# Kernel optimization log

Measured on AMD Instinct MI355X. Metric: run time of the kernel, lower is better.

The kernel has to match this reference:

```python
import jax, jax.numpy as jnp
import numpy as np

H, D_HEAD, MEM, K_OUT, J_DIM = 4, 16, 64, 192, 256
LN_EPS = 1e-5

def setup_inputs() -> dict:
    key = jax.random.key(0)
    ks = jax.random.split(key, 12)
    B, T, P = 4, 2048, 16
    inp = {
        "joint_repr": jax.random.normal(ks[0], (B, T, P, J_DIM), jnp.float32),
        "curvature": jax.random.uniform(ks[1], (B,), jnp.float32),
        "entropy": jax.random.uniform(ks[2], (B,), jnp.float32),
        "Wq": 0.02 * jax.random.normal(ks[3], (MEM, J_DIM), jnp.float32),
        "Wk": 0.02 * jax.random.normal(ks[4], (MEM, J_DIM), jnp.float32),
        "Wv": 0.02 * jax.random.normal(ks[5], (MEM, J_DIM), jnp.float32),
        "Wbeta_w": 0.05 * jax.random.normal(ks[6], (H, J_DIM), jnp.float32),
        "Wbeta_b": jnp.full((H,), 0.5, jnp.float32),
        "Walpha_w": 0.05 * jax.random.normal(ks[7], (H, J_DIM), jnp.float32),
        "Walpha_b": jnp.full((H,), -1.0, jnp.float32),
        "curv_w": 0.001 * jax.random.normal(ks[8], (H, 1), jnp.float32),
        "ent_w": 0.001 * jax.random.normal(ks[9], (H, 1), jnp.float32),
        "out_w": 0.01 * jax.random.normal(ks[10], (K_OUT, MEM), jnp.float32),
        "out_b": jnp.zeros((K_OUT,), jnp.float32),
        "ln_q_w": jnp.ones((D_HEAD,), jnp.float32),
        "ln_q_b": jnp.zeros((D_HEAD,), jnp.float32),
        "ln_k_w": jnp.ones((D_HEAD,), jnp.float32),
        "ln_k_b": jnp.zeros((D_HEAD,), jnp.float32),
    }
    return inp

def _ln(y, w, b):
    m = jnp.mean(y, axis=-1, keepdims=True)
    var = jnp.mean((y - m) ** 2, axis=-1, keepdims=True)
    return (y - m) / jnp.sqrt(var + LN_EPS) * w + b

def reference(joint_repr, curvature, entropy, Wq, Wk, Wv, Wbeta_w, Wbeta_b,
              Walpha_w, Walpha_b, curv_w, ent_w, out_w, out_b,
              ln_q_w, ln_q_b, ln_k_w, ln_k_b):
    B, T, P, J = joint_repr.shape
    N = B * P
    x = joint_repr.reshape(N, T, J)  # matches torch reshape(B*P, T, J)
    q = _ln((x @ Wq.T).reshape(N, T, H, D_HEAD), ln_q_w, ln_q_b)
    k = _ln((x @ Wk.T).reshape(N, T, H, D_HEAD), ln_k_w, ln_k_b)
    v = (x @ Wv.T).reshape(N, T, H, D_HEAD)
    k = k / jnp.clip(jnp.linalg.norm(k, axis=-1, keepdims=True), 1e-12)
    beta = jax.nn.sigmoid(x @ Wbeta_w.T + Wbeta_b)    # (N,T,H)
    alpha = jax.nn.sigmoid(x @ Walpha_w.T + Walpha_b)  # (N,T,H)
    # curvature modulation (detached in original)
    Kv = jnp.clip(jnp.abs(jax.lax.stop_gradient(curvature)), None, 10.0)
    Kv = jnp.repeat(Kv, P)  # (N,)
    beta = jax.nn.sigmoid(beta + Kv[:, None, None] * curv_w[:, 0])
    # entropy modulation (detached)
    Sv = jnp.clip(jax.lax.stop_gradient(entropy), 0.0, 5.0)
    Sv = jnp.repeat(Sv, P)
    alpha = jax.nn.sigmoid(alpha + Sv[:, None, None] * ent_w[:, 0])

    def step(M, inps):
        k_t, v_t, q_t, b_t, a_t = inps  # (N,H,d), (N,H)
        Mk = jnp.einsum('nhij,nhj->nhi', M, k_t)
        outer_kk = Mk[..., :, None] * k_t[..., None, :]
        outer_vk = v_t[..., :, None] * k_t[..., None, :]
        M = M - a_t[:, :, None, None] * outer_kk + b_t[:, :, None, None] * outer_vk
        o = jnp.einsum('nhij,nhj->nhi', M, q_t)
        return M, o

    M0 = jnp.zeros((N, H, D_HEAD, D_HEAD), joint_repr.dtype)
    xs = (k.transpose(1, 0, 2, 3), v.transpose(1, 0, 2, 3), q.transpose(1, 0, 2, 3),
          beta.transpose(1, 0, 2), alpha.transpose(1, 0, 2))
    _, outs = jax.lax.scan(step, M0, xs)  # (T,N,H,d)
    out = outs.transpose(1, 0, 2, 3).reshape(N, T, H * D_HEAD)
    fib = out @ out_w.T + out_b  # (N,T,K)
    return fib.reshape(B, P, T, K_OUT).transpose(0, 2, 1, 3)  # (B,T,P,K)
```

## Files before the change

### kernel.cpp

```cpp
#include <hip/hip_runtime.h>

#define TDIM 2048
#define SEG 16
#define SEGLEN 128

typedef __attribute__((ext_vector_type(8))) short short8;
typedef __attribute__((ext_vector_type(4))) short short4v;
typedef __attribute__((ext_vector_type(4))) float float4v;

__device__ __forceinline__ float sigf(float x) { return 1.0f / (1.0f + __expf(-x)); }

__device__ __forceinline__ unsigned short f2bf_rne(float f) {
    unsigned u = __float_as_uint(f);
    unsigned r = (u + 0x7fffu + ((u >> 16) & 1u)) >> 16;
    return (unsigned short)r;
}
__device__ __forceinline__ float bf2f(unsigned short h) {
    return __uint_as_float(((unsigned)h) << 16);
}
struct bfpair { short hi, lo; };
__device__ __forceinline__ bfpair cvt_split(float x) {
    bfpair p;
    unsigned short h = f2bf_rne(x);
    p.hi = (short)h;
    p.lo = (short)f2bf_rne(x - bf2f(h));
    return p;
}

__device__ __forceinline__ void split4_fast(float4 v, short4v& hi, short4v& lo) {
    unsigned h01, h23;
    asm("v_cvt_pk_bf16_f32 %0, %1, %2" : "=v"(h01) : "v"(v.x), "v"(v.y));
    asm("v_cvt_pk_bf16_f32 %0, %1, %2" : "=v"(h23) : "v"(v.z), "v"(v.w));
    float rx = v.x - __uint_as_float(h01 << 16);
    float ry = v.y - __uint_as_float(h01 & 0xffff0000u);
    float rz = v.z - __uint_as_float(h23 << 16);
    float rw = v.w - __uint_as_float(h23 & 0xffff0000u);
    unsigned l01, l23;
    asm("v_cvt_pk_bf16_f32 %0, %1, %2" : "=v"(l01) : "v"(rx), "v"(ry));
    asm("v_cvt_pk_bf16_f32 %0, %1, %2" : "=v"(l23) : "v"(rz), "v"(rw));
    union { unsigned u[2]; short4v s; } uh, ul;
    uh.u[0] = h01; uh.u[1] = h23;
    ul.u[0] = l01; ul.u[1] = l23;
    hi = uh.s; lo = ul.s;
}

template<int CTRL>
__device__ __forceinline__ float dpp_addt(float v) {
    int t = __builtin_amdgcn_update_dpp(0, __float_as_int(v), CTRL, 0xf, 0xf, true);
    return v + __int_as_float(t);
}
__device__ __forceinline__ float red16d(float v) {
    v = dpp_addt<0xB1>(v);
    v = dpp_addt<0x4E>(v);
    v = dpp_addt<0x141>(v);
    v = dpp_addt<0x140>(v);
    return v;
}

__device__ __forceinline__ float dot4f(float4 a, float4 b) {
    return fmaf(a.w, b.w, fmaf(a.z, b.z, fmaf(a.y, b.y, a.x * b.x)));
}
__device__ __forceinline__ float red4g(float v) {
    v += __shfl_xor(v, 16);
    v += __shfl_xor(v, 32);
    return v;
}

__device__ __forceinline__ void gld16(const void* g, void* l) {
    __builtin_amdgcn_global_load_lds(
        (const __attribute__((address_space(1))) unsigned*)g,
        (__attribute__((address_space(3))) unsigned*)l, 16, 0, 0);
}

__global__ __launch_bounds__(256) void prep_w_kernel(
    const float* __restrict__ Wq, const float* __restrict__ Wk, const float* __restrict__ Wv,
    const float* __restrict__ Wbw, const float* __restrict__ Waw,
    short* __restrict__ wimg)
{
    int u = blockIdx.x * 256 + threadIdx.x;
    if (u >= 6656) return;
    int kc = u / 1664, rem = u % 1664;
    int rr = rem >> 3, gg = rem & 7;
    const float* wrow = nullptr;
    if (rr < 64)       wrow = Wq  + (size_t)rr * 256;
    else if (rr < 128) wrow = Wk  + (size_t)(rr - 64) * 256;
    else if (rr < 192) wrow = Wv  + (size_t)(rr - 128) * 256;
    else if (rr < 196) wrow = Wbw + (size_t)(rr - 192) * 256;
    else if (rr < 200) wrow = Waw + (size_t)(rr - 196) * 256;
    int usw = (2 * gg) ^ (rr & 7);
    short* dh = wimg + ((size_t)kc * 3328 + rr * 16 + usw) * 8;
    short* dl = wimg + ((size_t)kc * 3328 + rr * 16 + (usw ^ 1)) * 8;
#pragma unroll
    for (int s = 0; s < 8; ++s) {
        float v = wrow ? wrow[kc * 64 + gg * 8 + s] : 0.0f;
        bfpair p = cvt_split(v);
        dh[s] = p.hi; dl[s] = p.lo;
    }
}

__global__ __launch_bounds__(256) void prep_ow_kernel(
    const float* __restrict__ ow, short* __restrict__ owimg)
{
    int u = blockIdx.x * 256 + threadIdx.x;
    if (u >= 1536) return;
    int rr = u >> 3, gg = u & 7;
    int usw = (2 * gg) ^ (rr & 7);
    short* dh = owimg + ((size_t)rr * 16 + usw) * 8;
    short* dl = owimg + ((size_t)rr * 16 + (usw ^ 1)) * 8;
#pragma unroll
    for (int s = 0; s < 8; ++s) {
        bfpair p = cvt_split(ow[(size_t)rr * 64 + gg * 8 + s]);
        dh[s] = p.hi; dl[s] = p.lo;
    }
}

__global__ __launch_bounds__(256, 2) void proj_kernel(
    const float* __restrict__ x, const float* __restrict__ curv, const float* __restrict__ ent,
    const short* __restrict__ wimg,
    const float* __restrict__ Wbb, const float* __restrict__ Wab,
    const float* __restrict__ cw, const float* __restrict__ ew,
    const float* __restrict__ lnqw, const float* __restrict__ lnqb,
    const float* __restrict__ lnkw, const float* __restrict__ lnkb,
    float* __restrict__ q_ws, float* __restrict__ k_ws, float* __restrict__ v_ws,
    float* __restrict__ beta_ws, float* __restrict__ alpha_ws)
{
    __shared__ __align__(16) short xsh[64 * 128];
    __shared__ __align__(16) short wsh[208 * 128];

    const int tid = threadIdx.x;
    const int lane = tid & 63, wv = tid >> 6;
    const int i16 = lane & 15, gq = lane >> 4, swz = i16 & 7;
    const int row0 = blockIdx.x * 64;
    const int ntbase = (wv == 0) ? 0 : (1 + 3 * wv);
    const int ntcnt  = (wv == 0) ? 4 : 3;

    float4v acc[4][4];
#pragma unroll
    for (int m = 0; m < 4; ++m)
#pragma unroll
        for (int nI = 0; nI < 4; ++nI) acc[m][nI] = (float4v){0.f, 0.f, 0.f, 0.f};

    float4 xr[4];
#pragma unroll
    for (int it = 0; it < 4; ++it) {
        int f = it * 256 + tid, rr = f >> 4, c4 = f & 15;
        xr[it] = *(const float4*)&x[(size_t)(row0 + rr) * 256 + c4 * 4];
    }

#pragma unroll
    for (int kc = 0; kc < 4; ++kc) {
        __builtin_amdgcn_s_barrier();
        const short* wsrc = wimg + (size_t)kc * 26624;
#pragma unroll
        for (int it = 0; it < 13; ++it) {
            int f = it * 256 + tid;
            gld16(wsrc + (size_t)f * 8, &wsh[f * 8]);
        }
        asm volatile("" ::: "memory");
#pragma unroll
        for (int it = 0; it < 4; ++it) {
            int f = it * 256 + tid, rr = f >> 4, c4 = f & 15;
            short4v hi, lo;
            split4_fast(xr[it], hi, lo);
            int usw = (2 * (c4 >> 1)) ^ (rr & 7);
            *(short4v*)&xsh[rr * 128 + usw * 8 + (c4 & 1) * 4] = hi;
            *(short4v*)&xsh[rr * 128 + (usw ^ 1) * 8 + (c4 & 1) * 4] = lo;
        }
        if (kc < 3) {
#pragma unroll
            for (int it = 0; it < 4; ++it) {
                int f = it * 256 + tid, rr = f >> 4, c4 = f & 15;
                xr[it] = *(const float4*)&x[(size_t)(row0 + rr) * 256 + (kc + 1) * 64 + c4 * 4];
            }
            asm volatile("s_waitcnt vmcnt(4) lgkmcnt(0)" ::: "memory");
        } else {
            asm volatile("s_waitcnt vmcnt(0) lgkmcnt(0)" ::: "memory");
        }
        __builtin_amdgcn_s_barrier();
#pragma unroll
        for (int ks = 0; ks < 2; ++ks) {
            const int g4 = ks * 4 + gq;
            const int uA = ((2 * g4) ^ swz) * 8;
            short8 ah[4], al[4];
#pragma unroll
            for (int m = 0; m < 4; ++m) {
                const int rb = (m * 16 + i16) * 128;
                ah[m] = *(const short8*)&xsh[rb + uA];
                al[m] = *(const short8*)&xsh[rb + (uA ^ 8)];
            }
#pragma unroll
            for (int nI = 0; nI < 4; ++nI) if (nI < ntcnt) {
                const int rowB = ((ntbase + nI) * 16 + i16) * 128;
                short8 bh = *(const short8*)&wsh[rowB + uA];
                short8 bl = *(const short8*)&wsh[rowB + (uA ^ 8)];
#pragma unroll
                for (int m = 0; m < 4; ++m) {
                    acc[m][nI] = __builtin_amdgcn_mfma_f32_16x16x32_bf16(ah[m], bh, acc[m][nI], 0, 0, 0);
                    acc[m][nI] = __builtin_amdgcn_mfma_f32_16x16x32_bf16(ah[m], bl, acc[m][nI], 0, 0, 0);
                    acc[m][nI] = __builtin_amdgcn_mfma_f32_16x16x32_bf16(al[m], bh, acc[m][nI], 0, 0, 0);
                }
            }
        }
    }

    const int c = i16;
    const float lnqw_c = lnqw[c], lnqb_c = lnqb[c];
    const float lnkw_c = lnkw[c], lnkb_c = lnkb[c];
    const int nblk = row0 >> 11;
    const float Kv = fminf(fabsf(curv[nblk >> 4]), 10.0f);
    const float Sv = fminf(fmaxf(ent[nblk >> 4], 0.0f), 5.0f);
#pragma unroll
    for (int nI = 0; nI < 4; ++nI) if (nI < ntcnt) {
        const int nt = ntbase + nI;
#pragma unroll
        for (int m = 0; m < 4; ++m) {
#pragma unroll
            for (int j = 0; j < 4; ++j) {
                const int grow = row0 + m * 16 + gq * 4 + j;
                const int n = grow >> 11, t = grow & 2047;
                float y = acc[m][nI][j];
                if (nt < 4) {
                    float s = red16d(y), s2 = red16d(y * y);
                    float mean = s * 0.0625f;
                    float var = s2 * 0.0625f - mean * mean;
                    float inv = rsqrtf(var + 1e-5f);
                    q_ws[((size_t)(n * 4 + nt) * TDIM + t) * 16 + c] = (y - mean) * inv * lnqw_c + lnqb_c;
                } else if (nt < 8) {
                    float s = red16d(y), s2 = red16d(y * y);
                    float mean = s * 0.0625f;
                    float var = s2 * 0.0625f - mean * mean;
                    float inv = rsqrtf(var + 1e-5f);
                    float kn = (y - mean) * inv * lnkw_c + lnkb_c;
                    float s3 = red16d(kn * kn);
                    kn = kn / fmaxf(sqrtf(s3), 1e-12f);
                    k_ws[((size_t)(n * 4 + (nt - 4)) * TDIM + t) * 16 + c] = kn;
                } else if (nt < 12) {
                    v_ws[((size_t)(n * 4 + (nt - 8)) * TDIM + t) * 16 + c] = y;
                } else {
                    if (c < 4)
                        beta_ws[(size_t)(n * 4 + c) * TDIM + t] = sigf(sigf(y + Wbb[c]) + Kv * cw[c]);
                    else if (c < 8) {
                        int h = c - 4;
                        alpha_ws[(size_t)(n * 4 + h) * TDIM + t] = sigf(sigf(y + Wab[h]) + Sv * ew[h]);
                    }
                }
            }
        }
    }
}

__global__ __launch_bounds__(64) void scan_p1_kernel(
    const float* __restrict__ k_ws, const float* __restrict__ v_ws,
    const float* __restrict__ beta_ws, const float* __restrict__ alpha_ws,
    float* __restrict__ pq_ws)
{
    __shared__ __align__(16) float ks[128 * 16], bvs[128 * 16];
    __shared__ __align__(16) float tb1[128 * 4];
    const int tid = threadIdx.x;
    const int sid = blockIdx.x;
    const int cid = blockIdx.y;
    const int i = tid & 15, g = tid >> 4;
    const int t0g = sid * SEGLEN;
    const float* kb = k_ws + ((size_t)cid * TDIM + t0g) * 16;
    const float* vb = v_ws + ((size_t)cid * TDIM + t0g) * 16;
    const float* bb = beta_ws + (size_t)cid * TDIM + t0g;
    const float* ab = alpha_ws + (size_t)cid * TDIM + t0g;

    for (int f = tid; f < 128 * 16; f += 64) { ks[f] = 0.f; bvs[f] = 0.f; }
    for (int f = tid; f < 128 * 4; f += 64) tb1[f] = 0.f;
    __syncthreads();

    float4 kr[4], vr[4]; float be = 0.f, alp = 0.f;
    auto load_stage = [&](int s) {
        size_t t0 = (size_t)s * 64 + tid;
        const float4* kp = (const float4*)(kb + t0 * 16);
        const float4* vp = (const float4*)(vb + t0 * 16);
#pragma unroll
        for (int j = 0; j < 4; ++j) { kr[j] = kp[j]; vr[j] = vp[j]; }
        be = bb[t0]; alp = ab[t0];
    };
    auto commit_stage = [&](int s) {
        int r = (s & 1) * 64 + tid;
#pragma unroll
        for (int j = 0; j < 4; ++j) {
            *(float4*)&ks[r * 16 + 4 * j] = kr[j];
            float4 bv4 = make_float4(be * vr[j].x, be * vr[j].y, be * vr[j].z, be * vr[j].w);
            *(float4*)&bvs[r * 16 + 4 * j] = bv4;
        }
    };
    auto table_pass = [&](int s) {
        int r0 = (s & 1) * 64 + tid;
        int rm1 = (r0 - 1) & 127, rm2 = (r0 - 2) & 127;
        float C = 0.f, C2 = 0.f;
#pragma unroll
        for (int j = 0; j < 4; ++j) {
            float4 kt  = *(float4*)&ks[r0 * 16 + 4 * j];
            float4 km1 = *(float4*)&ks[rm1 * 16 + 4 * j];
            float4 km2 = *(float4*)&ks[rm2 * 16 + 4 * j];
            C  += dot4f(km1, kt);
            C2 += dot4f(km2, kt);
        }
        *(float4*)&tb1[r0 * 4] = make_float4(alp * C, alp * C2, alp, 0.f);
    };

    load_stage(0);
    commit_stage(0);
    __syncthreads();
    table_pass(0);
    __syncthreads();

    float4 Q4 = make_float4(0.f, 0.f, 0.f, 0.f);
    float4 P4 = make_float4(i == 4 * g + 0 ? 1.f : 0.f,
                            i == 4 * g + 1 ? 1.f : 0.f,
                            i == 4 * g + 2 ? 1.f : 0.f,
                            i == 4 * g + 3 ? 1.f : 0.f);
    float wq1 = 0.f, wq2 = 0.f, wp1 = 0.f, wp2 = 0.f;
    float4 k4m1 = make_float4(0.f, 0.f, 0.f, 0.f);
    float4 k4_0 = *(float4*)&ks[0 * 16 + 4 * g];
    float4 k4p1 = *(float4*)&ks[1 * 16 + 4 * g];
    float upQ_cur = 0.f;
    float upP_cur = ks[i];
    float4 ta0 = *(float4*)&tb1[0];
    float aC1_c = ta0.x, aC2_c = ta0.y, al_c = ta0.z;
    float bv_c = bvs[i];

    int t = 0;
    auto step = [&]() {
        int rp2 = (t + 2) & 127, rp1 = (t + 1) & 127;
        float4 k4in = *(float4*)&ks[rp2 * 16 + 4 * g];
        float4 tain = *(float4*)&tb1[rp1 * 4];
        float bvin = bvs[rp1 * 16 + i];
        float upQ = red4g(dot4f(Q4, k4p1));
        float upP = red4g(dot4f(P4, k4p1));
        Q4.x = fmaf(wq1, k4m1.x, Q4.x);
        Q4.y = fmaf(wq1, k4m1.y, Q4.y);
        Q4.z = fmaf(wq1, k4m1.z, Q4.z);
        Q4.w = fmaf(wq1, k4m1.w, Q4.w);
        P4.x = fmaf(wp1, k4m1.x, P4.x);
        P4.y = fmaf(wp1, k4m1.y, P4.y);
        P4.z = fmaf(wp1, k4m1.z, P4.z);
        P4.w = fmaf(wp1, k4m1.w, P4.w);
        float rq = fmaf(-aC2_c, wq2, fmaf(-al_c, upQ_cur, bv_c));
        float wq0 = fmaf(-aC1_c, wq1, rq);
        float rp_ = fmaf(-aC2_c, wp2, -al_c * upP_cur);
        float wp0 = fmaf(-aC1_c, wp1, rp_);
        wq2 = wq1; wq1 = wq0; wp2 = wp1; wp1 = wp0;
        k4m1 = k4_0; k4_0 = k4p1; k4p1 = k4in;
        upQ_cur = upQ; upP_cur = upP;
        aC1_c = tain.x; aC2_c = tain.y; al_c = tain.z; bv_c = bvin;
        ++t;
    };

    load_stage(1);
#pragma unroll 4
    for (int u = 0; u < 32; ++u) step();
    commit_stage(1);
#pragma unroll 4
    for (int u = 0; u < 16; ++u) step();
    table_pass(1);
#pragma unroll 4
    for (int u = 0; u < 16; ++u) step();
#pragma unroll 4
    for (int u = 0; u < 64; ++u) step();

    Q4.x = fmaf(wq1, k4m1.x, Q4.x);
    Q4.y = fmaf(wq1, k4m1.y, Q4.y);
    Q4.z = fmaf(wq1, k4m1.z, Q4.z);
    Q4.w = fmaf(wq1, k4m1.w, Q4.w);
    P4.x = fmaf(wp1, k4m1.x, P4.x);
    P4.y = fmaf(wp1, k4m1.y, P4.y);
    P4.z = fmaf(wp1, k4m1.z, P4.z);
    P4.w = fmaf(wp1, k4m1.w, P4.w);

    float* dst = pq_ws + ((size_t)cid * 15 + sid) * 512;
    *(float4*)&dst[i * 16 + 4 * g] = Q4;
    *(float4*)&dst[256 + i * 16 + 4 * g] = P4;
}

__global__ __launch_bounds__(64) void scan_p2_kernel(
    const float* __restrict__ pq_ws, float* __restrict__ min_ws)
{
    __shared__ float Mlds[256], Plds[256];
    const int tid = threadIdx.x;
    const int cid = blockIdx.x;
    const int i = tid & 15, g = tid >> 4;
    float4 M4 = make_float4(0.f, 0.f, 0.f, 0.f);
    *(float4*)&min_ws[((size_t)cid * SEG + 0) * 256 + i * 16 + 4 * g] = M4;
    for (int sid = 0; sid < 15; ++sid) {
        const float* base = pq_ws + ((size_t)cid * 15 + sid) * 512;
        float4 Qn = *(const float4*)&base[i * 16 + 4 * g];
        float4 Pn = *(const float4*)&base[256 + i * 16 + 4 * g];
        *(float4*)&Mlds[i * 16 + 4 * g] = M4;
        *(float4*)&Plds[i * 16 + 4 * g] = Pn;
        __syncthreads();
        float4 acc = Qn;
#pragma unroll
        for (int m = 0; m < 16; ++m) {
            float mm = Mlds[i * 16 + m];
            float4 pr = *(float4*)&Plds[m * 16 + 4 * g];
            acc.x = fmaf(mm, pr.x, acc.x);
            acc.y = fmaf(mm, pr.y, acc.y);
            acc.z = fmaf(mm, pr.z, acc.z);
            acc.w = fmaf(mm, pr.w, acc.w);
        }
        M4 = acc;
        __syncthreads();
        *(float4*)&min_ws[((size_t)cid * SEG + sid + 1) * 256 + i * 16 + 4 * g] = M4;
    }
}

__global__ __launch_bounds__(64) void scan_p3_kernel(
    const float* __restrict__ q_ws, const float* __restrict__ k_ws, const float* __restrict__ v_ws,
    const float* __restrict__ beta_ws, const float* __restrict__ alpha_ws,
    const float* __restrict__ min_ws, float* __restrict__ o_ws)
{
    __shared__ __align__(16) float ks[128 * 16], qs[128 * 16], bvs[128 * 16];
    __shared__ __align__(16) float tbl[128 * 8];
    __shared__ __align__(16) float os[64 * 16];
    const int tid = threadIdx.x;
    const int sid = blockIdx.x;
    const int cid = blockIdx.y;
    const int i = tid & 15, g = tid >> 4;
    const int t0g = sid * SEGLEN;
    const float* kb = k_ws + ((size_t)cid * TDIM + t0g) * 16;
    const float* qb = q_ws + ((size_t)cid * TDIM + t0g) * 16;
    const float* vb = v_ws + ((size_t)cid * TDIM + t0g) * 16;
    const float* bb = beta_ws + (size_t)cid * TDIM + t0g;
    const float* ab = alpha_ws + (size_t)cid * TDIM + t0g;
    float* obp = o_ws + ((size_t)cid * TDIM + t0g) * 16;

    for (int f = tid; f < 128 * 16; f += 64) { ks[f] = 0.f; qs[f] = 0.f; bvs[f] = 0.f; }
    for (int f = tid; f < 128 * 8; f += 64) tbl[f] = 0.f;
    __syncthreads();

    float4 kr[4], qr[4], vr[4]; float be = 0.f, alp = 0.f;
    auto load_stage = [&](int s) {
        size_t t0 = (size_t)s * 64 + tid;
        const float4* kp = (const float4*)(kb + t0 * 16);
        const float4* qp = (const float4*)(qb + t0 * 16);
        const float4* vp = (const float4*)(vb + t0 * 16);
#pragma unroll
        for (int j = 0; j < 4; ++j) { kr[j] = kp[j]; qr[j] = qp[j]; vr[j] = vp[j]; }
        be = bb[t0]; alp = ab[t0];
    };
    auto commit_stage = [&](int s) {
        int r = (s & 1) * 64 + tid;
#pragma unroll
        for (int j = 0; j < 4; ++j) {
            *(float4*)&ks[r * 16 + 4 * j] = kr[j];
            *(float4*)&qs[r * 16 + 4 * j] = qr[j];
            float4 bv4 = make_float4(be * vr[j].x, be * vr[j].y, be * vr[j].z, be * vr[j].w);
            *(float4*)&bvs[r * 16 + 4 * j] = bv4;
        }
    };
    auto table_pass = [&](int s) {
        int r0 = (s & 1) * 64 + tid;
        int rm1 = (r0 - 1) & 127, rm2 = (r0 - 2) & 127;
        float C = 0.f, C2 = 0.f, d = 0.f, e = 0.f, E2 = 0.f;
#pragma unroll
        for (int j = 0; j < 4; ++j) {
            float4 kt  = *(float4*)&ks[r0 * 16 + 4 * j];
            float4 km1 = *(float4*)&ks[rm1 * 16 + 4 * j];
            float4 km2 = *(float4*)&ks[rm2 * 16 + 4 * j];
            float4 qt  = *(float4*)&qs[r0 * 16 + 4 * j];
            C  += dot4f(km1, kt);
            C2 += dot4f(km2, kt);
            d  += dot4f(kt,  qt);
            e  += dot4f(km1, qt);
            E2 += dot4f(km2, qt);
        }
        *(float4*)&tbl[r0 * 8] = make_float4(alp * C, alp * C2, d, e);
        *(float2*)&tbl[r0 * 8 + 4] = make_float2(E2, alp);
    };

    load_stage(0);
    commit_stage(0);
    __syncthreads();
    table_pass(0);
    __syncthreads();

    float4 M4 = *(const float4*)&min_ws[((size_t)cid * SEG + sid) * 256 + i * 16 + 4 * g];
    float w1 = 0.f, w2 = 0.f;
    float4 k4m1 = make_float4(0.f, 0.f, 0.f, 0.f);
    float4 k4_0 = *(float4*)&ks[0 * 16 + 4 * g];
    float4 q4_0 = *(float4*)&qs[0 * 16 + 4 * g];
    float4 k4p1 = *(float4*)&ks[1 * 16 + 4 * g];
    float4 q4p1 = *(float4*)&qs[1 * 16 + 4 * g];
    float up_cur = red4g(dot4f(M4, k4_0));
    float rp_cur = red4g(dot4f(M4, q4_0));
    float4 ta0 = *(float4*)&tbl[0];
    float aC1_c = ta0.x, aC2_c = ta0.y, d_c = ta0.z, e_c = ta0.w;
    float2 tx0 = *(float2*)&tbl[4];
    float E2_c = tx0.x, al_c = tx0.y;
    float bv_c = bvs[i];

    int t = 0;
    auto step = [&]() {
        int rp2 = (t + 2) & 127, rp1 = (t + 1) & 127;
        float4 k4in = *(float4*)&ks[rp2 * 16 + 4 * g];
        float4 q4in = *(float4*)&qs[rp2 * 16 + 4 * g];
        float4 tain = *(float4*)&tbl[rp1 * 8];
        float2 txin = *(float2*)&tbl[rp1 * 8 + 4];
        float bvin = bvs[rp1 * 16 + i];
        float up = red4g(dot4f(M4, k4p1));
        float rp = red4g(dot4f(M4, q4p1));
        M4.x = fmaf(w1, k4m1.x, M4.x);
        M4.y = fmaf(w1, k4m1.y, M4.y);
        M4.z = fmaf(w1, k4m1.z, M4.z);
        M4.w = fmaf(w1, k4m1.w, M4.w);
        float r = fmaf(-aC2_c, w2, fmaf(-al_c, up_cur, bv_c));
        float w0 = fmaf(-aC1_c, w1, r);
        float o = fmaf(w0, d_c, fmaf(w1, e_c, fmaf(w2, E2_c, rp_cur)));
        if (g == 0) os[(t & 63) * 16 + i] = o;
        w2 = w1; w1 = w0;
        k4m1 = k4_0; k4_0 = k4p1; k4p1 = k4in;
        q4p1 = q4in;
        up_cur = up; rp_cur = rp;
        aC1_c = tain.x; aC2_c = tain.y; d_c = tain.z; e_c = tain.w;
        E2_c = txin.x; al_c = txin.y; bv_c = bvin;
        ++t;
    };

    for (int s = 0; s < 2; ++s) {
        if (s == 0) load_stage(1);
#pragma unroll 4
        for (int u = 0; u < 32; ++u) step();
        if (s == 0) commit_stage(1);
#pragma unroll 4
        for (int u = 0; u < 16; ++u) step();
        if (s == 0) table_pass(1);
#pragma unroll 4
        for (int u = 0; u < 16; ++u) step();
#pragma unroll
        for (int j = 0; j < 4; ++j) {
            float4 ov = *(float4*)&os[(tid * 4 + j) * 4];
            *(float4*)&obp[(size_t)s * 1024 + (tid * 4 + j) * 4] = ov;
        }
    }
}

__global__ __launch_bounds__(256, 2) void outproj_kernel(
    const float* __restrict__ o_ws, const short* __restrict__ owimg,
    const float* __restrict__ ob, float* __restrict__ out)
{
    __shared__ __align__(16) short osh[64 * 128];
    __shared__ __align__(16) short wsh[192 * 128];
    const int tid = threadIdx.x;
    const int lane = tid & 63, wv = tid >> 6;
    const int i16 = lane & 15, gq = lane >> 4, swz = i16 & 7;
    const int row0 = blockIdx.x * 64;
    const int ntbase = wv * 3;

    float4v acc[4][3];
#pragma unroll
    for (int m = 0; m < 4; ++m)
#pragma unroll
        for (int nI = 0; nI < 3; ++nI) acc[m][nI] = (float4v){0.f, 0.f, 0.f, 0.f};

#pragma unroll
    for (int it = 0; it < 12; ++it) {
        int f = it * 256 + tid;
        gld16(owimg + (size_t)f * 8, &wsh[f * 8]);
    }
    asm volatile("" ::: "memory");
#pragma unroll
    for (int it = 0; it < 4; ++it) {
        int f = it * 256 + tid, rr = f >> 4, c4 = f & 15;
        int grow = row0 + rr;
        int n = grow >> 11, t = grow & 2047;
        int h = c4 >> 2, d4 = c4 & 3;
        float4 xv = *(const float4*)&o_ws[((size_t)(n * 4 + h) * TDIM + t) * 16 + d4 * 4];
        short4v hi, lo;
        split4_fast(xv, hi, lo);
        int usw = (2 * (c4 >> 1)) ^ (rr & 7);
        *(short4v*)&osh[rr * 128 + usw * 8 + (c4 & 1) * 4] = hi;
        *(short4v*)&osh[rr * 128 + (usw ^ 1) * 8 + (c4 & 1) * 4] = lo;
    }
    __syncthreads();

#pragma unroll
    for (int ks = 0; ks < 2; ++ks) {
        const int g4 = ks * 4 + gq;
        const int uA = ((2 * g4) ^ swz) * 8;
        short8 ah[4], al[4];
#pragma unroll
        for (int m = 0; m < 4; ++m) {
            const int rb = (m * 16 + i16) * 128;
            ah[m] = *(const short8*)&osh[rb + uA];
            al[m] = *(const short8*)&osh[rb + (uA ^ 8)];
        }
#pragma unroll
        for (int nI = 0; nI < 3; ++nI) {
            const int rowB = ((ntbase + nI) * 16 + i16) * 128;
            short8 bh = *(const short8*)&wsh[rowB + uA];
            short8 bl = *(const short8*)&wsh[rowB + (uA ^ 8)];
#pragma unroll
            for (int m = 0; m < 4; ++m) {
                acc[m][nI] = __builtin_amdgcn_mfma_f32_16x16x32_bf16(ah[m], bh, acc[m][nI], 0, 0, 0);
                acc[m][nI] = __builtin_amdgcn_mfma_f32_16x16x32_bf16(ah[m], bl, acc[m][nI], 0, 0, 0);
                acc[m][nI] = __builtin_amdgcn_mfma_f32_16x16x32_bf16(al[m], bh, acc[m][nI], 0, 0, 0);
            }
        }
    }

#pragma unroll
    for (int nI = 0; nI < 3; ++nI) {
        const int nt = ntbase + nI;
        const float bias = ob[nt * 16 + i16];
#pragma unroll
        for (int m = 0; m < 4; ++m) {
#pragma unroll
            for (int j = 0; j < 4; ++j) {
                int grow = row0 + m * 16 + gq * 4 + j;
                int n = grow >> 11, t = grow & 2047;
                int b = n >> 4, p = n & 15;
                out[((size_t)(b * TDIM + t) * 16 + p) * 192 + nt * 16 + i16] = acc[m][nI][j] + bias;
            }
        }
    }
}

extern "C" void kernel_launch(void* const* d_in, const int* in_sizes, int n_in,
                              void* d_out, int out_size, void* d_ws, size_t ws_size,
                              hipStream_t stream) {
    (void)in_sizes; (void)n_in; (void)out_size; (void)ws_size;
    const float* x    = (const float*)d_in[0];
    const float* curv = (const float*)d_in[1];
    const float* ent  = (const float*)d_in[2];
    const float* Wq   = (const float*)d_in[3];
    const float* Wk   = (const float*)d_in[4];
    const float* Wv   = (const float*)d_in[5];
    const float* Wbw  = (const float*)d_in[6];
    const float* Wbb  = (const float*)d_in[7];
    const float* Waw  = (const float*)d_in[8];
    const float* Wab  = (const float*)d_in[9];
    const float* cw   = (const float*)d_in[10];
    const float* ew   = (const float*)d_in[11];
    const float* ow   = (const float*)d_in[12];
    const float* ob   = (const float*)d_in[13];
    const float* lnqw = (const float*)d_in[14];
    const float* lnqb = (const float*)d_in[15];
    const float* lnkw = (const float*)d_in[16];
    const float* lnkb = (const float*)d_in[17];
    float* out = (float*)d_out;

    float* ws = (float*)d_ws;
    float* q_ws     = ws;
    float* k_ws     = q_ws + 8388608;
    float* v_ws     = k_ws + 8388608;
    float* beta_ws  = v_ws + 8388608;
    float* alpha_ws = beta_ws + 524288;
    float* o_ws     = alpha_ws + 524288;

    short* wimg  = (short*)o_ws;
    short* owimg = (short*)q_ws;
    float* pq_ws  = out;
    float* min_ws = out + 1966080;

    prep_w_kernel<<<26, 256, 0, stream>>>(Wq, Wk, Wv, Wbw, Waw, wimg);
    proj_kernel<<<2048, 256, 0, stream>>>(x, curv, ent, wimg, Wbb, Wab,
                                          cw, ew, lnqw, lnqb, lnkw, lnkb,
                                          q_ws, k_ws, v_ws, beta_ws, alpha_ws);
    scan_p1_kernel<<<dim3(15, 256), 64, 0, stream>>>(k_ws, v_ws, beta_ws, alpha_ws, pq_ws);
    scan_p2_kernel<<<256, 64, 0, stream>>>(pq_ws, min_ws);
    scan_p3_kernel<<<dim3(16, 256), 64, 0, stream>>>(q_ws, k_ws, v_ws, beta_ws, alpha_ws,
                                                     min_ws, o_ws);
    prep_ow_kernel<<<6, 256, 0, stream>>>(ow, owimg);
    outproj_kernel<<<2048, 256, 0, stream>>>(o_ws, owimg, ob, out);
}
```

Baseline: 512.9 us.

## Halve K-chunk size in projection kernels to fit four blocks per CU

The proj and outproj kernels now stage half-width K chunks (32 columns instead of 64) through LDS, which roughly halves shared memory per block. Launch bounds are raised from 2 to 4 blocks per CU to take advantage of the smaller footprint. Each kernel now runs twice as many load/barrier/compute iterations. The tighter launch bound also caps registers per thread, which risks spilling of the accumulator arrays.

```diff
diff --git a/kernel.cpp b/kernel.cpp
--- a/kernel.cpp
+++ b/kernel.cpp
@@ -114,7 +114,7 @@
     }
 }
 
-__global__ __launch_bounds__(256, 2) void proj_kernel(
+__global__ __launch_bounds__(256, 4) void proj_kernel(
     const float* __restrict__ x, const float* __restrict__ curv, const float* __restrict__ ent,
     const short* __restrict__ wimg,
     const float* __restrict__ Wbb, const float* __restrict__ Wab,
@@ -124,8 +124,8 @@
     float* __restrict__ q_ws, float* __restrict__ k_ws, float* __restrict__ v_ws,
     float* __restrict__ beta_ws, float* __restrict__ alpha_ws)
 {
-    __shared__ __align__(16) short xsh[64 * 128];
-    __shared__ __align__(16) short wsh[208 * 128];
+    __shared__ __align__(16) short xsh[64 * 64];
+    __shared__ __align__(16) short wsh[1664 * 8];
 
     const int tid = threadIdx.x;
     const int lane = tid & 63, wv = tid >> 6;
@@ -140,65 +140,64 @@
 #pragma unroll
         for (int nI = 0; nI < 4; ++nI) acc[m][nI] = (float4v){0.f, 0.f, 0.f, 0.f};
 
-    float4 xr[4];
-#pragma unroll
-    for (int it = 0; it < 4; ++it) {
-        int f = it * 256 + tid, rr = f >> 4, c4 = f & 15;
+    float4 xr[2];
+#pragma unroll
+    for (int it = 0; it < 2; ++it) {
+        int f = it * 256 + tid, rr = f >> 3, c4 = f & 7;
         xr[it] = *(const float4*)&x[(size_t)(row0 + rr) * 256 + c4 * 4];
     }
 
-#pragma unroll
-    for (int kc = 0; kc < 4; ++kc) {
+    for (int hc = 0; hc < 8; ++hc) {
         __builtin_amdgcn_s_barrier();
-        const short* wsrc = wimg + (size_t)kc * 26624;
-#pragma unroll
-        for (int it = 0; it < 13; ++it) {
+        const short* wk = wimg + (size_t)(hc >> 1) * 26624;
+        const int hoff = (hc & 1) * 8;
+#pragma unroll
+        for (int it = 0; it < 7; ++it) {
             int f = it * 256 + tid;
-            gld16(wsrc + (size_t)f * 8, &wsh[f * 8]);
+            if (f < 1664) {
+                int rr = f >> 3, uu = f & 7;
+                gld16(wk + ((size_t)rr * 16 + hoff + uu) * 8, &wsh[f * 8]);
+            }
         }
         asm volatile("" ::: "memory");
 #pragma unroll
-        for (int it = 0; it < 4; ++it) {
-            int f = it * 256 + tid, rr = f >> 4, c4 = f & 15;
+        for (int it = 0; it < 2; ++it) {
+            int f = it * 256 + tid, rr = f >> 3, c4 = f & 7;
             short4v hi, lo;
             split4_fast(xr[it], hi, lo);
             int usw = (2 * (c4 >> 1)) ^ (rr & 7);
-            *(short4v*)&xsh[rr * 128 + usw * 8 + (c4 & 1) * 4] = hi;
-            *(short4v*)&xsh[rr * 128 + (usw ^ 1) * 8 + (c4 & 1) * 4] = lo;
-        }
-        if (kc < 3) {
-#pragma unroll
-            for (int it = 0; it < 4; ++it) {
-                int f = it * 256 + tid, rr = f >> 4, c4 = f & 15;
-                xr[it] = *(const float4*)&x[(size_t)(row0 + rr) * 256 + (kc + 1) * 64 + c4 * 4];
+            *(short4v*)&xsh[rr * 64 + usw * 8 + (c4 & 1) * 4] = hi;
+            *(short4v*)&xsh[rr * 64 + (usw ^ 1) * 8 + (c4 & 1) * 4] = lo;
+        }
+        if (hc < 7) {
+#pragma unroll
+            for (int it = 0; it < 2; ++it) {
+                int f = it * 256 + tid, rr = f >> 3, c4 = f & 7;
+                xr[it] = *(const float4*)&x[(size_t)(row0 + rr) * 256 + (hc + 1) * 32 + c4 * 4];
             }
-            asm volatile("s_waitcnt vmcnt(4) lgkmcnt(0)" ::: "memory");
+            asm volatile("s_waitcnt vmcnt(2) lgkmcnt(0)" ::: "memory");
         } else {
             asm volatile("s_waitcnt vmcnt(0) lgkmcnt(0)" ::: "memory");
         }
         __builtin_amdgcn_s_barrier();
-#pragma unroll
-        for (int ks = 0; ks < 2; ++ks) {
-            const int g4 = ks * 4 + gq;
-            const int uA = ((2 * g4) ^ swz) * 8;
-            short8 ah[4], al[4];
+        const int uA = ((2 * gq) ^ swz) * 8;
+        short8 ah[4], al[4];
+#pragma unroll
+        for (int m = 0; m < 4; ++m) {
+            const int rb = (m * 16 + i16) * 64;
+            ah[m] = *(const short8*)&xsh[rb + uA];
+            al[m] = *(const short8*)&xsh[rb + (uA ^ 8)];
+        }
+#pragma unroll
+        for (int nI = 0; nI < 4; ++nI) if (nI < ntcnt) {
+            const int rowB = ((ntbase + nI) * 16 + i16) * 64;
+            short8 bh = *(const short8*)&wsh[rowB + uA];
+            short8 bl = *(const short8*)&wsh[rowB + (uA ^ 8)];
 #pragma unroll
             for (int m = 0; m < 4; ++m) {
-                const int rb = (m * 16 + i16) * 128;
-                ah[m] = *(const short8*)&xsh[rb + uA];
-                al[m] = *(const short8*)&xsh[rb + (uA ^ 8)];
-            }
-#pragma unroll
-            for (int nI = 0; nI < 4; ++nI) if (nI < ntcnt) {
-                const int rowB = ((ntbase + nI) * 16 + i16) * 128;
-                short8 bh = *(const short8*)&wsh[rowB + uA];
-                short8 bl = *(const short8*)&wsh[rowB + (uA ^ 8)];
-#pragma unroll
-                for (int m = 0; m < 4; ++m) {
-                    acc[m][nI] = __builtin_amdgcn_mfma_f32_16x16x32_bf16(ah[m], bh, acc[m][nI], 0, 0, 0);
-                    acc[m][nI] = __builtin_amdgcn_mfma_f32_16x16x32_bf16(ah[m], bl, acc[m][nI], 0, 0, 0);
-                    acc[m][nI] = __builtin_amdgcn_mfma_f32_16x16x32_bf16(al[m], bh, acc[m][nI], 0, 0, 0);
-                }
+                acc[m][nI] = __builtin_amdgcn_mfma_f32_16x16x32_bf16(ah[m], bh, acc[m][nI], 0, 0, 0);
+                acc[m][nI] = __builtin_amdgcn_mfma_f32_16x16x32_bf16(ah[m], bl, acc[m][nI], 0, 0, 0);
+                acc[m][nI] = __builtin_amdgcn_mfma_f32_16x16x32_bf16(al[m], bh, acc[m][nI], 0, 0, 0);
             }
         }
     }
@@ -539,12 +538,12 @@
     }
 }
 
-__global__ __launch_bounds__(256, 2) void outproj_kernel(
+__global__ __launch_bounds__(256, 4) void outproj_kernel(
     const float* __restrict__ o_ws, const short* __restrict__ owimg,
     const float* __restrict__ ob, float* __restrict__ out)
 {
-    __shared__ __align__(16) short osh[64 * 128];
-    __shared__ __align__(16) short wsh[192 * 128];
+    __shared__ __align__(16) short osh[64 * 64];
+    __shared__ __align__(16) short wsh[1536 * 8];
     const int tid = threadIdx.x;
     const int lane = tid & 63, wv = tid >> 6;
     const int i16 = lane & 15, gq = lane >> 4, swz = i16 & 7;
@@ -557,41 +556,62 @@
 #pragma unroll
         for (int nI = 0; nI < 3; ++nI) acc[m][nI] = (float4v){0.f, 0.f, 0.f, 0.f};
 
-#pragma unroll
-    for (int it = 0; it < 12; ++it) {
-        int f = it * 256 + tid;
-        gld16(owimg + (size_t)f * 8, &wsh[f * 8]);
-    }
-    asm volatile("" ::: "memory");
-#pragma unroll
-    for (int it = 0; it < 4; ++it) {
-        int f = it * 256 + tid, rr = f >> 4, c4 = f & 15;
+    float4 orr[2];
+#pragma unroll
+    for (int it = 0; it < 2; ++it) {
+        int f = it * 256 + tid, rr = f >> 3, c4 = f & 7;
         int grow = row0 + rr;
         int n = grow >> 11, t = grow & 2047;
         int h = c4 >> 2, d4 = c4 & 3;
-        float4 xv = *(const float4*)&o_ws[((size_t)(n * 4 + h) * TDIM + t) * 16 + d4 * 4];
-        short4v hi, lo;
-        split4_fast(xv, hi, lo);
-        int usw = (2 * (c4 >> 1)) ^ (rr & 7);
-        *(short4v*)&osh[rr * 128 + usw * 8 + (c4 & 1) * 4] = hi;
-        *(short4v*)&osh[rr * 128 + (usw ^ 1) * 8 + (c4 & 1) * 4] = lo;
-    }
-    __syncthreads();
-
-#pragma unroll
-    for (int ks = 0; ks < 2; ++ks) {
-        const int g4 = ks * 4 + gq;
-        const int uA = ((2 * g4) ^ swz) * 8;
+        orr[it] = *(const float4*)&o_ws[((size_t)(n * 4 + h) * TDIM + t) * 16 + d4 * 4];
+    }
+
+#pragma unroll
+    for (int half = 0; half < 2; ++half) {
+        __builtin_amdgcn_s_barrier();
+#pragma unroll
+        for (int it = 0; it < 6; ++it) {
+            int f = it * 256 + tid;
+            int rr = f >> 3, uu = f & 7;
+            gld16(owimg + ((size_t)rr * 16 + half * 8 + uu) * 8, &wsh[f * 8]);
+        }
+        asm volatile("" ::: "memory");
+#pragma unroll
+        for (int it = 0; it < 2; ++it) {
+            int f = it * 256 + tid, rr = f >> 3, c4 = f & 7;
+            short4v hi, lo;
+            split4_fast(orr[it], hi, lo);
+            int usw = (2 * (c4 >> 1)) ^ (rr & 7);
+            *(short4v*)&osh[rr * 64 + usw * 8 + (c4 & 1) * 4] = hi;
+            *(short4v*)&osh[rr * 64 + (usw ^ 1) * 8 + (c4 & 1) * 4] = lo;
+        }
+        if (half == 0) {
+#pragma unroll
+            for (int it = 0; it < 2; ++it) {
+                int f = it * 256 + tid, rr = f >> 3, c4 = f & 7;
+                int grow = row0 + rr;
+                int n = grow >> 11, t = grow & 2047;
+                int col = 32 + c4 * 4;
+                int h = col >> 4, d4 = (col >> 2) & 3;
+                orr[it] = *(const float4*)&o_ws[((size_t)(n * 4 + h) * TDIM + t) * 16 + d4 * 4];
+            }
+            asm volatile("s_waitcnt vmcnt(2) lgkmcnt(0)" ::: "memory");
+        } else {
+            asm volatile("s_waitcnt vmcnt(0) lgkmcnt(0)" ::: "memory");
+        }
+        __builtin_amdgcn_s_barrier();
+
+        const int uA = ((2 * gq) ^ swz) * 8;
         short8 ah[4], al[4];
 #pragma unroll
         for (int m = 0; m < 4; ++m) {
-            const int rb = (m * 16 + i16) * 128;
+            const int rb = (m * 16 + i16) * 64;
             ah[m] = *(const short8*)&osh[rb + uA];
             al[m] = *(const short8*)&osh[rb + (uA ^ 8)];
         }
 #pragma unroll
         for (int nI = 0; nI < 3; ++nI) {
-            const int rowB = ((ntbase + nI) * 16 + i16) * 128;
+            const int rowB = ((ntbase + nI) * 16 + i16) * 64;
             short8 bh = *(const short8*)&wsh[rowB + uA];
             short8 bl = *(const short8*)&wsh[rowB + (uA ^ 8)];
 #pragma unroll
```

Measured after the change: 516.2 us. About the same (+0.6%).
